# Kernel tuning notes

Hardware: AMD Instinct MI355X
Metric: run time of the kernel (lower is better)

## Reference

```python
import jax, jax.numpy as jnp
import numpy as np

B, T = 2048, 32          # batch, max utterance length
V, H, A = 32000, 1024, 1000  # vocab, embedding_size, num_actions


def setup_inputs() -> dict:
    key = jax.random.key(0)
    ks = jax.random.split(key, 6)
    s = 0.02
    return {
        "utterance": jax.random.randint(ks[0], (B, T), 0, V, dtype=jnp.int32),
        "global_idxes": jnp.arange(B, dtype=jnp.int32),
        "emb_w": jax.random.normal(ks[1], (V, H), jnp.float32) * s,
        "w_ih": jax.random.normal(ks[2], (3 * H, H), jnp.float32) * s,
        "w_hh": jax.random.normal(ks[3], (3 * H, H), jnp.float32) * s,
        "b_ih": jnp.zeros((3 * H,), jnp.float32),
        "b_hh": jnp.zeros((3 * H,), jnp.float32),
        "h1_w": jax.random.normal(ks[4], (A, H), jnp.float32) * s,
        "h1_b": jnp.zeros((A,), jnp.float32),
    }


def _gru_cell(x, h, w_ih, w_hh, b_ih, b_hh):
    # PyTorch GRUCell: gate order r, z, n along the 3H axis
    gi = x @ w_ih.T + b_ih   # [B, 3H]
    gh = h @ w_hh.T + b_hh   # [B, 3H]
    ir, iz, inn = jnp.split(gi, 3, axis=-1)
    hr, hz, hn = jnp.split(gh, 3, axis=-1)
    r = jax.nn.sigmoid(ir + hr)
    z = jax.nn.sigmoid(iz + hz)
    n = jnp.tanh(inn + r * hn)
    return (1.0 - z) * n + z * h


def reference(utterance, global_idxes, emb_w, w_ih, w_hh, b_ih, b_hh, h1_w, h1_b):
    # Sieve semantics: a row stays alive until it emits token 0; the state is
    # updated at the step where the 0 token is consumed (inclusive), then frozen.
    batch = utterance.shape[0]
    hdim = emb_w.shape[1]

    def step(carry, tok_t):
        state, alive = carry
        emb = emb_w[tok_t]                              # [B, H] embedding lookup
        new_state = _gru_cell(emb, state, w_ih, w_hh, b_ih, b_hh)
        state = jnp.where(alive[:, None], new_state, state)
        alive = alive & (tok_t != 0)
        return (state, alive), None

    init = (jnp.zeros((batch, hdim), emb_w.dtype), jnp.ones((batch,), bool))
    (state, _), _ = jax.lax.scan(step, init, utterance.T)  # scan over time

    action_logits = state @ h1_w.T + h1_b                  # [B, A]
    action_probs = jax.nn.softmax(action_logits, axis=-1)
    return action_probs
```

## Files before the change

kernel.cpp:

```cpp
#include <hip/hip_runtime.h>
#include <cstdint>
#include <cstddef>

#define B_  2048
#define T_  32
#define V_  32000
#define H_  1024
#define A_  1000
#define H3  3072

typedef short short8 __attribute__((ext_vector_type(8)));
typedef float f32x4  __attribute__((ext_vector_type(4)));

typedef __attribute__((address_space(1))) void* as1v;
typedef __attribute__((address_space(3))) void* as3v;

__device__ __forceinline__ unsigned short f2bf(float f) {
  union { float f; unsigned u; } v; v.f = f;
  unsigned r = v.u + 0x7FFFu + ((v.u >> 16) & 1u);
  return (unsigned short)(r >> 16);
}
__device__ __forceinline__ float bf2f(unsigned short s) {
  union { unsigned u; float f; } v; v.u = ((unsigned)s) << 16;
  return v.f;
}
__device__ __forceinline__ float sigmoidf(float x) {
  return 1.f / (1.f + __expf(-x));
}


__global__ void conv_bf16(const float* __restrict__ src, unsigned short* __restrict__ dst, int n4) {
  int i = blockIdx.x * blockDim.x + threadIdx.x;
  if (i >= n4) return;
  float4 v = ((const float4*)src)[i];
  ushort4 o;
  o.x = f2bf(v.x); o.y = f2bf(v.y); o.z = f2bf(v.z); o.w = f2bf(v.w);
  ((ushort4*)dst)[i] = o;
}

__global__ void conv_h1w(const float* __restrict__ src, unsigned short* __restrict__ dst) {
  int i = blockIdx.x * blockDim.x + threadIdx.x;
  if (i >= 1024 * 1024) return;
  int row = i >> 10;
  dst[i] = (row < A_) ? f2bf(src[i]) : (unsigned short)0;
}

__global__ void init_state(float* __restrict__ state, unsigned short* __restrict__ hbf0) {
  int i = blockIdx.x * blockDim.x + threadIdx.x;
  if (i < B_ * H_) { state[i] = 0.f; hbf0[i] = 0; }
}

__global__ void prep(const int* __restrict__ utt, unsigned* __restrict__ alivemask,
                     int* __restrict__ uttT) {
  int b = blockIdx.x * blockDim.x + threadIdx.x;
  if (b >= B_) return;
  unsigned mask = 0, alive = 1;
  #pragma unroll
  for (int t = 0; t < T_; t++) {
    int tk = utt[b * T_ + t];
    mask |= alive << t;
    if (tk == 0) alive = 0;
    uttT[t * B_ + b] = tk;
  }
  alivemask[b] = mask;
}

__global__ void __launch_bounds__(256) gemm_ew(
    const unsigned short* __restrict__ Abase,
    const unsigned short* __restrict__ W,
    const float* __restrict__ bias,
    unsigned short* __restrict__ Cw)
{
  __shared__ __align__(16) unsigned short lA[128 * 64];
  __shared__ __align__(16) unsigned short lB[128 * 64];
  const int tid  = threadIdx.x;
  const int lane = tid & 63;
  const int wv   = tid >> 6;
  const int wr   = (wv >> 1) * 64;
  const int wc   = (wv & 1) * 64;
  const int lm   = lane & 15;
  const int lq   = lane >> 4;
  const int bx   = blockIdx.x, by = blockIdx.y;

  f32x4 acc[4][4];
  #pragma unroll
  for (int i = 0; i < 4; i++)
    #pragma unroll
    for (int j = 0; j < 4; j++)
      acc[i][j] = (f32x4){0.f, 0.f, 0.f, 0.f};

  for (int kt = 0; kt < H_; kt += 64) {
    __syncthreads();
    #pragma unroll
    for (int r = 0; r < 4; r++) {
      int li  = r * 256 + tid;
      int row = li >> 3;
      int gc  = (li & 7) ^ (row & 7);
      const unsigned short* ga = Abase + (size_t)(by * 128 + row) * H_ + kt + gc * 8;
      __builtin_amdgcn_global_load_lds((as1v)ga, (as3v)(&lA[(size_t)li * 8]), 16, 0, 0);
      const unsigned short* gb = W + (size_t)(bx * 128 + row) * H_ + kt + gc * 8;
      __builtin_amdgcn_global_load_lds((as1v)gb, (as3v)(&lB[(size_t)li * 8]), 16, 0, 0);
    }
    __syncthreads();
    #pragma unroll
    for (int kk = 0; kk < 2; kk++) {
      const int cs = (((kk << 2) | lq) ^ (lm & 7)) << 3;
      short8 af[4], bf[4];
      #pragma unroll
      for (int i = 0; i < 4; i++)
        af[i] = *(const short8*)&lA[(wr + i * 16 + lm) * 64 + cs];
      #pragma unroll
      for (int j = 0; j < 4; j++)
        bf[j] = *(const short8*)&lB[(wc + j * 16 + lm) * 64 + cs];
      #pragma unroll
      for (int i = 0; i < 4; i++)
        #pragma unroll
        for (int j = 0; j < 4; j++)
          acc[i][j] = __builtin_amdgcn_mfma_f32_16x16x32_bf16(af[i], bf[j], acc[i][j], 0, 0, 0);
    }
  }
  #pragma unroll
  for (int i = 0; i < 4; i++) {
    int row0 = by * 128 + wr + i * 16 + lq * 4;
    #pragma unroll
    for (int j = 0; j < 4; j++) {
      int col = bx * 128 + wc + j * 16 + lm;
      float bv = bias[col];
      #pragma unroll
      for (int rg = 0; rg < 4; rg++)
        Cw[(size_t)(row0 + rg) * H3 + col] = f2bf(acc[i][j][rg] + bv);
    }
  }
}

__global__ void __launch_bounds__(256) gemm_final(
    const unsigned short* __restrict__ Abase,
    const unsigned short* __restrict__ W,
    float* __restrict__ C)
{
  __shared__ __align__(16) unsigned short lA[128 * 64];
  __shared__ __align__(16) unsigned short lB[128 * 64];
  const int tid  = threadIdx.x;
  const int lane = tid & 63;
  const int wv   = tid >> 6;
  const int wr   = (wv >> 1) * 64;
  const int wc   = (wv & 1) * 64;
  const int lm   = lane & 15;
  const int lq   = lane >> 4;
  const int bx   = blockIdx.x, by = blockIdx.y;

  f32x4 acc[4][4];
  #pragma unroll
  for (int i = 0; i < 4; i++)
    #pragma unroll
    for (int j = 0; j < 4; j++)
      acc[i][j] = (f32x4){0.f, 0.f, 0.f, 0.f};

  for (int kt = 0; kt < H_; kt += 64) {
    __syncthreads();
    #pragma unroll
    for (int r = 0; r < 4; r++) {
      int li  = r * 256 + tid;
      int row = li >> 3;
      int gc  = (li & 7) ^ (row & 7);
      const unsigned short* ga = Abase + (size_t)(by * 128 + row) * H_ + kt + gc * 8;
      __builtin_amdgcn_global_load_lds((as1v)ga, (as3v)(&lA[(size_t)li * 8]), 16, 0, 0);
      const unsigned short* gb = W + (size_t)(bx * 128 + row) * H_ + kt + gc * 8;
      __builtin_amdgcn_global_load_lds((as1v)gb, (as3v)(&lB[(size_t)li * 8]), 16, 0, 0);
    }
    __syncthreads();
    #pragma unroll
    for (int kk = 0; kk < 2; kk++) {
      const int cs = (((kk << 2) | lq) ^ (lm & 7)) << 3;
      short8 af[4], bf[4];
      #pragma unroll
      for (int i = 0; i < 4; i++)
        af[i] = *(const short8*)&lA[(wr + i * 16 + lm) * 64 + cs];
      #pragma unroll
      for (int j = 0; j < 4; j++)
        bf[j] = *(const short8*)&lB[(wc + j * 16 + lm) * 64 + cs];
      #pragma unroll
      for (int i = 0; i < 4; i++)
        #pragma unroll
        for (int j = 0; j < 4; j++)
          acc[i][j] = __builtin_amdgcn_mfma_f32_16x16x32_bf16(af[i], bf[j], acc[i][j], 0, 0, 0);
    }
  }
  #pragma unroll
  for (int i = 0; i < 4; i++) {
    int row0 = by * 128 + wr + i * 16 + lq * 4;
    #pragma unroll
    for (int j = 0; j < 4; j++) {
      int col = bx * 128 + wc + j * 16 + lm;
      #pragma unroll
      for (int rg = 0; rg < 4; rg++)
        C[(size_t)(row0 + rg) * 1024 + col] = acc[i][j][rg];
    }
  }
}

__global__ void __launch_bounds__(256, 4) step_fused(
    const unsigned short* __restrict__ EW,
    const int* __restrict__ uttT, int t,
    const unsigned short* __restrict__ hin,
    const unsigned short* __restrict__ whh_bf,
    const float* __restrict__ bhh,
    float* __restrict__ state,
    unsigned short* __restrict__ hout,
    const unsigned* __restrict__ amask)
{
  __shared__ __align__(16) unsigned short lA[2][64 * 64];
  __shared__ __align__(16) unsigned short lB[2][3 * 32 * 64];

  const int tid  = threadIdx.x;
  const int lane = tid & 63;
  const int wv   = tid >> 6;
  const int lm   = lane & 15;
  const int lq   = lane >> 4;
  const int hx   = blockIdx.x;
  const int bb   = blockIdx.y;

  auto STAGE = [&](int buf, int kt) {
    #pragma unroll
    for (int it = 0; it < 2; it++) {
      int li  = it * 256 + tid;
      int row = li >> 3;
      int gc  = (li & 7) ^ (row & 7);
      const unsigned short* ga = hin + (size_t)(bb * 64 + row) * H_ + kt + gc * 8;
      __builtin_amdgcn_global_load_lds((as1v)ga, (as3v)(&lA[buf][(size_t)li * 8]), 16, 0, 0);
    }
    #pragma unroll
    for (int gg = 0; gg < 3; gg++) {
      int li  = gg * 256 + tid;
      int g   = li >> 8;
      int row = (li >> 3) & 31;
      int gc  = (li & 7) ^ (row & 7);
      const unsigned short* gb = whh_bf + (size_t)((g << 10) + hx * 32 + row) * H_ + kt + gc * 8;
      __builtin_amdgcn_global_load_lds((as1v)gb, (as3v)(&lB[buf][(size_t)li * 8]), 16, 0, 0);
    }
  };

  STAGE(0, 0);

  int tokr[4];
  #pragma unroll
  for (int rg = 0; rg < 4; rg++)
    tokr[rg] = uttT[t * B_ + bb * 64 + wv * 16 + lq * 4 + rg];

  float hreg[2][4];
  float gir[2][4], giz[2][4], gin[2][4];
  #pragma unroll
  for (int j = 0; j < 2; j++) {
    int col = hx * 32 + j * 16 + lm;
    #pragma unroll
    for (int rg = 0; rg < 4; rg++) {
      int row = bb * 64 + wv * 16 + lq * 4 + rg;
      hreg[j][rg] = state[(size_t)row * H_ + col];
      const unsigned short* ep = EW + (size_t)tokr[rg] * H3 + col;
      gir[j][rg] = bf2f(ep[0]);
      giz[j][rg] = bf2f(ep[H_]);
      gin[j][rg] = bf2f(ep[2 * H_]);
    }
  }

  f32x4 acc[3][2];
  #pragma unroll
  for (int g = 0; g < 3; g++)
    #pragma unroll
    for (int j = 0; j < 2; j++)
      acc[g][j] = (f32x4){0.f, 0.f, 0.f, 0.f};

  #pragma unroll 1
  for (int kti = 0; kti < 16; kti++) {
    const int cur = kti & 1;
    __builtin_amdgcn_s_barrier();
    __builtin_amdgcn_sched_barrier(0);
    if (kti < 15) {
      STAGE(cur ^ 1, (kti + 1) * 64);
      asm volatile("s_waitcnt vmcnt(5)" ::: "memory");
    } else {
      asm volatile("s_waitcnt vmcnt(0)" ::: "memory");
    }
    __builtin_amdgcn_sched_barrier(0);
    __builtin_amdgcn_s_barrier();
    __builtin_amdgcn_sched_barrier(0);
    #pragma unroll
    for (int kk = 0; kk < 2; kk++) {
      const int cs = (((kk << 2) | lq) ^ (lm & 7)) << 3;
      short8 af = *(const short8*)&lA[cur][(wv * 16 + lm) * 64 + cs];
      #pragma unroll
      for (int g = 0; g < 3; g++) {
        #pragma unroll
        for (int j = 0; j < 2; j++) {
          short8 bf = *(const short8*)&lB[cur][g * 2048 + (j * 16 + lm) * 64 + cs];
          acc[g][j] = __builtin_amdgcn_mfma_f32_16x16x32_bf16(af, bf, acc[g][j], 0, 0, 0);
        }
      }
    }
  }

  #pragma unroll
  for (int j = 0; j < 2; j++) {
    int col = hx * 32 + j * 16 + lm;
    float bhr = bhh[col];
    float bhz = bhh[H_ + col];
    float bhn = bhh[2 * H_ + col];
    #pragma unroll
    for (int rg = 0; rg < 4; rg++) {
      int row = bb * 64 + wv * 16 + lq * 4 + rg;
      float r = sigmoidf(gir[j][rg] + acc[0][j][rg] + bhr);
      float z = sigmoidf(giz[j][rg] + acc[1][j][rg] + bhz);
      float n = tanhf(gin[j][rg] + r * (acc[2][j][rg] + bhn));
      float h = hreg[j][rg];
      float nh = (1.f - z) * n + z * h;
      float o = ((amask[row] >> t) & 1u) ? nh : h;
      size_t si = (size_t)row * H_ + col;
      state[si] = o;
      hout[si] = f2bf(o);
    }
  }
}

__global__ void __launch_bounds__(256) softmax_k(const float* __restrict__ logits,
                                                 const float* __restrict__ h1b,
                                                 float* __restrict__ out)
{
  int b = blockIdx.x;
  int tid = threadIdx.x;
  __shared__ float red[8];
  float v[4];
  float lmax = -3.4e38f;
  #pragma unroll
  for (int k = 0; k < 4; k++) {
    int j = tid + k * 256;
    float x = (j < A_) ? (logits[(size_t)b * 1024 + j] + h1b[j]) : -3.4e38f;
    v[k] = x;
    lmax = fmaxf(lmax, x);
  }
  #pragma unroll
  for (int off = 1; off < 64; off <<= 1) lmax = fmaxf(lmax, __shfl_xor(lmax, off, 64));
  if ((tid & 63) == 0) red[tid >> 6] = lmax;
  __syncthreads();
  lmax = fmaxf(fmaxf(red[0], red[1]), fmaxf(red[2], red[3]));
  float s = 0.f;
  #pragma unroll
  for (int k = 0; k < 4; k++) {
    int j = tid + k * 256;
    float e = (j < A_) ? expf(v[k] - lmax) : 0.f;
    v[k] = e; s += e;
  }
  #pragma unroll
  for (int off = 1; off < 64; off <<= 1) s += __shfl_xor(s, off, 64);
  if ((tid & 63) == 0) red[4 + (tid >> 6)] = s;
  __syncthreads();
  s = red[4] + red[5] + red[6] + red[7];
  float inv = 1.f / s;
  #pragma unroll
  for (int k = 0; k < 4; k++) {
    int j = tid + k * 256;
    if (j < A_) out[(size_t)b * A_ + j] = v[k] * inv;
  }
}

extern "C" void kernel_launch(void* const* d_in, const int* in_sizes, int n_in,
                              void* d_out, int out_size, void* d_ws, size_t ws_size,
                              hipStream_t stream)
{
  (void)in_sizes; (void)n_in; (void)out_size; (void)ws_size;
  const int*   utt   = (const int*)d_in[0];
  const float* emb_w = (const float*)d_in[2];
  const float* w_ih  = (const float*)d_in[3];
  const float* w_hh  = (const float*)d_in[4];
  const float* b_ih  = (const float*)d_in[5];
  const float* b_hh  = (const float*)d_in[6];
  const float* h1_w  = (const float*)d_in[7];
  const float* h1_b  = (const float*)d_in[8];
  float* out = (float*)d_out;

  char* ws = (char*)d_ws;
  size_t off = 0;
  auto alloc = [&](size_t bytes) {
    void* p = ws + off;
    off += (bytes + 255) & ~(size_t)255;
    return p;
  };
  unsigned short* emb_bf = (unsigned short*)alloc((size_t)V_ * H_ * 2);
  unsigned short* wih_bf = (unsigned short*)alloc((size_t)H3 * H_ * 2);
  unsigned short* EW     = (unsigned short*)alloc((size_t)V_ * H3 * 2);
  unsigned short* whh_bf = (unsigned short*)alloc((size_t)H3 * H_ * 2);
  int*            uttT   = (int*)alloc((size_t)B_ * T_ * 4);
  unsigned*       amask  = (unsigned*)alloc((size_t)B_ * 4);

  char* ov = (char*)emb_bf;
  unsigned short* h1w_bf = (unsigned short*)(ov);
  float*          state  = (float*)(ov + 2097152);
  unsigned short* hbf0   = (unsigned short*)(ov + 10485760);
  unsigned short* hbf1   = (unsigned short*)(ov + 14680064);
  float*          logits = (float*)(ov + 18874368);

  int n4 = V_ * H_ / 4;
  conv_bf16<<<(n4 + 255) / 256, 256, 0, stream>>>(emb_w, emb_bf, n4);
  n4 = H3 * H_ / 4;
  conv_bf16<<<(n4 + 255) / 256, 256, 0, stream>>>(w_ih, wih_bf, n4);
  conv_bf16<<<(n4 + 255) / 256, 256, 0, stream>>>(w_hh, whh_bf, n4);
  prep<<<(B_ + 255) / 256, 256, 0, stream>>>(utt, amask, uttT);

  dim3 gew(H3 / 128, V_ / 128);
  gemm_ew<<<gew, 256, 0, stream>>>(emb_bf, wih_bf, b_ih, EW);

  conv_h1w<<<(1024 * 1024) / 256, 256, 0, stream>>>(h1_w, h1w_bf);
  init_state<<<(B_ * H_) / 256, 256, 0, stream>>>(state, hbf0);

  unsigned short* hb[2] = { hbf0, hbf1 };
  dim3 gst(32, 32);
  for (int t = 0; t < T_; t++) {
    step_fused<<<gst, 256, 0, stream>>>(EW, uttT, t, hb[t & 1], whh_bf, b_hh,
                                        state, hb[(t + 1) & 1], amask);
  }
  dim3 gf(1024 / 128, B_ / 128);
  gemm_final<<<gf, 256, 0, stream>>>(hb[0], h1w_bf, logits);
  softmax_k<<<B_, 256, 0, stream>>>(logits, h1_b, out);
}
```

Baseline: 1.333 ms.

## Double-buffer LDS tiles in input-projection GEMM to overlap loads with MFMA

Splits the LDS A/B tiles into two buffers so the global-to-LDS loads for the next K tile are issued before the MFMAs on the current tile run. Uses explicit s_waitcnt vmcnt and barriers to wait only for the current tile's loads. This hides global memory latency in the gemm_ew kernel, at the cost of twice the shared memory per block, which may lower occupancy.

```diff
diff --git a/kernel.cpp b/kernel.cpp
--- a/kernel.cpp
+++ b/kernel.cpp
@@ -71,8 +71,8 @@
     const float* __restrict__ bias,
     unsigned short* __restrict__ Cw)
 {
-  __shared__ __align__(16) unsigned short lA[128 * 64];
-  __shared__ __align__(16) unsigned short lB[128 * 64];
+  __shared__ __align__(16) unsigned short lA[2][128 * 64];
+  __shared__ __align__(16) unsigned short lB[2][128 * 64];
   const int tid  = threadIdx.x;
   const int lane = tid & 63;
   const int wv   = tid >> 6;
@@ -89,29 +89,45 @@
     for (int j = 0; j < 4; j++)
       acc[i][j] = (f32x4){0.f, 0.f, 0.f, 0.f};
 
-  for (int kt = 0; kt < H_; kt += 64) {
-    __syncthreads();
+  auto STAGE = [&](int buf, int kt) {
     #pragma unroll
     for (int r = 0; r < 4; r++) {
       int li  = r * 256 + tid;
       int row = li >> 3;
       int gc  = (li & 7) ^ (row & 7);
       const unsigned short* ga = Abase + (size_t)(by * 128 + row) * H_ + kt + gc * 8;
-      __builtin_amdgcn_global_load_lds((as1v)ga, (as3v)(&lA[(size_t)li * 8]), 16, 0, 0);
+      __builtin_amdgcn_global_load_lds((as1v)ga, (as3v)(&lA[buf][(size_t)li * 8]), 16, 0, 0);
       const unsigned short* gb = W + (size_t)(bx * 128 + row) * H_ + kt + gc * 8;
-      __builtin_amdgcn_global_load_lds((as1v)gb, (as3v)(&lB[(size_t)li * 8]), 16, 0, 0);
-    }
-    __syncthreads();
+      __builtin_amdgcn_global_load_lds((as1v)gb, (as3v)(&lB[buf][(size_t)li * 8]), 16, 0, 0);
+    }
+  };
+
+  STAGE(0, 0);
+
+  #pragma unroll 1
+  for (int kti = 0; kti < 16; kti++) {
+    const int cur = kti & 1;
+    __builtin_amdgcn_s_barrier();
+    __builtin_amdgcn_sched_barrier(0);
+    if (kti < 15) {
+      STAGE(cur ^ 1, (kti + 1) * 64);
+      asm volatile("s_waitcnt vmcnt(8)" ::: "memory");
+    } else {
+      asm volatile("s_waitcnt vmcnt(0)" ::: "memory");
+    }
+    __builtin_amdgcn_sched_barrier(0);
+    __builtin_amdgcn_s_barrier();
+    __builtin_amdgcn_sched_barrier(0);
     #pragma unroll
     for (int kk = 0; kk < 2; kk++) {
       const int cs = (((kk << 2) | lq) ^ (lm & 7)) << 3;
       short8 af[4], bf[4];
       #pragma unroll
       for (int i = 0; i < 4; i++)
-        af[i] = *(const short8*)&lA[(wr + i * 16 + lm) * 64 + cs];
+        af[i] = *(const short8*)&lA[cur][(wr + i * 16 + lm) * 64 + cs];
       #pragma unroll
       for (int j = 0; j < 4; j++)
-        bf[j] = *(const short8*)&lB[(wc + j * 16 + lm) * 64 + cs];
+        bf[j] = *(const short8*)&lB[cur][(wc + j * 16 + lm) * 64 + cs];
       #pragma unroll
       for (int i = 0; i < 4; i++)
         #pragma unroll
```

Measured after the change: 1.309 ms. Within noise of the previous version (-1.8%).
